# Performance work log

Hardware: AMD Instinct MI355X
Metric: run time of the kernel (lower is better)

Reference implementation:

```python
import jax, jax.numpy as jnp
import numpy as np

N = 20000        # nodes
E = 160000       # directed edges (before self loops)
NODE_DIM = 1287
HEADS = 4
C1, C2, C3 = 128, 256, 128
ACT_SLOPE = 0.15   # module's LeakyReLU between layers
GAT_SLOPE = 0.2    # PyG GATConv default negative_slope


def _gat_layer(x, src, dst, W, att_src, att_dst, bias, heads, out_dim, concat):
    # x: [N, in] ; W: [in, heads*out] ; att_*: [heads, out] ; bias: [heads*out] or [out]
    h = (x @ W).reshape(N, heads, out_dim)                      # [N, H, C]
    a_s = jnp.einsum('nhc,hc->nh', h, att_src)                  # [N, H]
    a_d = jnp.einsum('nhc,hc->nh', h, att_dst)                  # [N, H]
    e = jax.nn.leaky_relu(a_s[src] + a_d[dst], GAT_SLOPE)       # [Etot, H]
    # segment softmax over incoming edges of each dst node (self loops => no empty segments)
    m = jax.ops.segment_max(e, dst, num_segments=N)             # [N, H]
    w = jnp.exp(e - m[dst])
    den = jax.ops.segment_sum(w, dst, num_segments=N)           # [N, H]
    alpha = w / den[dst]                                        # [Etot, H]
    msg = h[src] * alpha[:, :, None]                            # [Etot, H, C]
    out = jax.ops.segment_sum(msg, dst, num_segments=N)         # [N, H, C]
    out = out.reshape(N, heads * out_dim) if concat else out.mean(axis=1)
    return out + bias


def setup_inputs() -> dict:
    key = jax.random.key(0)
    ks = jax.random.split(key, 22)
    s = 0.05
    x = jax.random.normal(ks[0], (N, NODE_DIM), jnp.float32)
    edge_index = jax.random.randint(ks[1], (2, E), 0, N, dtype=jnp.int64)
    inp = {
        'x': x, 'edge_index': edge_index,
        'W1': jax.random.normal(ks[2], (NODE_DIM, HEADS * C1), jnp.float32) * s,
        'as1': jax.random.normal(ks[3], (HEADS, C1), jnp.float32) * s,
        'ad1': jax.random.normal(ks[4], (HEADS, C1), jnp.float32) * s,
        'b1': jnp.zeros((HEADS * C1,), jnp.float32),
        'W2': jax.random.normal(ks[5], (HEADS * C1, HEADS * C2), jnp.float32) * s,
        'as2': jax.random.normal(ks[6], (HEADS, C2), jnp.float32) * s,
        'ad2': jax.random.normal(ks[7], (HEADS, C2), jnp.float32) * s,
        'b2': jnp.zeros((HEADS * C2,), jnp.float32),
        # conv3: 1024 -> 128, 1 head, no concat
        'W3': jax.random.normal(ks[8], (HEADS * C2, C3), jnp.float32) * s,
        'as3': jax.random.normal(ks[9], (1, C3), jnp.float32) * s,
        'ad3': jax.random.normal(ks[10], (1, C3), jnp.float32) * s,
        'b3': jnp.zeros((C3,), jnp.float32),
        # pre_fc: 128 -> 16
        'pw': jax.random.normal(ks[11], (C3, 16), jnp.float32) * s,
        'pb': jnp.zeros((16,), jnp.float32),
        # fc fallback: Linear(16,32) -> LeakyReLU(0.15) -> Linear(32,2)
        'f1w': jax.random.normal(ks[12], (16, 32), jnp.float32) * s,
        'f1b': jnp.zeros((32,), jnp.float32),
        'f2w': jax.random.normal(ks[13], (32, 2), jnp.float32) * s,
        'f2b': jnp.zeros((2,), jnp.float32),
    }
    return inp


def reference(x, edge_index, W1, as1, ad1, b1, W2, as2, ad2, b2,
              W3, as3, ad3, b3, pw, pb, f1w, f1b, f2w, f2b):
    loop = jnp.arange(N, dtype=edge_index.dtype)
    src = jnp.concatenate([edge_index[0], loop])   # PyG add_self_loops=True
    dst = jnp.concatenate([edge_index[1], loop])
    h = _gat_layer(x, src, dst, W1, as1, ad1, b1, HEADS, C1, True)
    h = jax.nn.leaky_relu(h, ACT_SLOPE)            # dropout = identity (eval)
    h = _gat_layer(h, src, dst, W2, as2, ad2, b2, HEADS, C2, True)
    h = jax.nn.leaky_relu(h, ACT_SLOPE)
    h = _gat_layer(h, src, dst, W3, as3, ad3, b3, 1, C3, False)
    h = jax.nn.leaky_relu(h, ACT_SLOPE)
    h = h @ pw + pb                                 # pre_fc (128 -> 16)
    h = jax.nn.leaky_relu(h @ f1w + f1b, ACT_SLOPE)
    return h @ f2w + f2b                            # [N, 2] logits
```

## Files before the change

kernel.cpp:

```cpp
#include <hip/hip_runtime.h>
#include <hip/hip_bf16.h>
#include <cstdint>
#include <cstddef>

#define LRELU(x, s) ((x) > 0.f ? (x) : (s) * (x))

typedef __attribute__((ext_vector_type(8))) short bf16x8;
typedef __attribute__((ext_vector_type(4))) float f32x4;

__device__ __forceinline__ float bflo(uint v) { return __uint_as_float(v << 16); }
__device__ __forceinline__ float bfhi(uint v) { return __uint_as_float(v & 0xffff0000u); }
__device__ __forceinline__ ushort f2bf(float f) {
  const uint u = __float_as_uint(f);
  return (ushort)((u + 0x7fffu + ((u >> 16) & 1u)) >> 16);
}

__device__ __forceinline__ void async16(const ushort* g, ushort* l) {
  __builtin_amdgcn_global_load_lds(
      (const __attribute__((address_space(1))) unsigned int*)g,
      (__attribute__((address_space(3))) unsigned int*)l, 16, 0, 0);
}

#define WAITCNT_VM(n) (0xF70 | (n))

__global__ void cast_pad_rows(const float* __restrict__ in, ushort* __restrict__ out,
                              int rows, int K, int Kp) {
  const int P4 = Kp >> 2;
  const long long idx = (long long)blockIdx.x * blockDim.x + threadIdx.x;
  if (idx >= (long long)rows * P4) return;
  const int r = (int)(idx / P4);
  const int c = ((int)(idx - (long long)r * P4)) << 2;
  const float* p = in + (size_t)r * K + c;
  float v0 = 0.f, v1 = 0.f, v2 = 0.f, v3 = 0.f;
  if (c + 3 < K) { v0 = p[0]; v1 = p[1]; v2 = p[2]; v3 = p[3]; }
  else {
    if (c + 0 < K) v0 = p[0];
    if (c + 1 < K) v1 = p[1];
    if (c + 2 < K) v2 = p[2];
    if (c + 3 < K) v3 = p[3];
  }
  uint2 o;
  o.x = (uint)f2bf(v0) | ((uint)f2bf(v1) << 16);
  o.y = (uint)f2bf(v2) | ((uint)f2bf(v3) << 16);
  *(uint2*)(out + (size_t)r * Kp + c) = o;
}

__global__ void cast_W_T(const float* __restrict__ W, ushort* __restrict__ Wt,
                         int K, int Nn, int Kp) {
  __shared__ float tile[32][33];
  const int kt = blockIdx.x * 32;
  const int nt = blockIdx.y * 32;
  const int tx = threadIdx.x;
  const int ty = threadIdx.y;
  for (int r = ty; r < 32; r += 8) {
    const int k = kt + r, nn = nt + tx;
    tile[r][tx] = (k < K && nn < Nn) ? W[(size_t)k * Nn + nn] : 0.f;
  }
  __syncthreads();
  for (int r = ty; r < 32; r += 8) {
    const int nn = nt + r, k = kt + tx;
    if (nn < Nn && k < Kp) Wt[(size_t)nn * Kp + k] = f2bf(tile[tx][r]);
  }
}

template <int TM>
__global__ __launch_bounds__(256) void gemm_bf16(
    const ushort* __restrict__ A, const ushort* __restrict__ Bt, ushort* __restrict__ C,
    int M, int N, int Kp,
    const float* __restrict__ AS, const float* __restrict__ AD,
    float* __restrict__ asb, float* __restrict__ adb, int H, int headC) {
  constexpr int MI = TM / 32;
  constexpr int LPG = (TM == 128) ? 4 : 3;
  __shared__ ushort sA[2 * TM * 32];
  __shared__ ushort sB[2 * 128 * 32];
  const int tid = threadIdx.x;
  const int wave = tid >> 6;
  const int lane = tid & 63;
  const int tilesN = N >> 7;
  const int bx = blockIdx.x % tilesN;
  const int by = blockIdx.x / tilesN;
  const int wrow = (wave >> 1) * (TM / 2);
  const int wcol = (wave & 1) * 64;
  const int quad = lane >> 4;
  const int ml = lane & 15;

  const int seg = (lane & 3) * 8;
  const int rB0 = wave * 32 + (lane >> 2);
  const int gB0 = bx * 128 + rB0;
  const ushort* pB0 = Bt + (size_t)gB0 * Kp + seg;
  const ushort* pB1 = Bt + (size_t)(gB0 + 16) * Kp + seg;
  ushort* lB0 = &sB[(wave * 32) * 32];
  ushort* lB1 = &sB[(wave * 32 + 16) * 32];
  const ushort *pA0, *pA1;
  ushort *lA0, *lA1;
  if constexpr (TM == 128) {
    const int r0 = wave * 32 + (lane >> 2);
    pA0 = A + (size_t)min(by * TM + r0, M - 1) * Kp + seg;
    pA1 = A + (size_t)min(by * TM + r0 + 16, M - 1) * Kp + seg;
    lA0 = &sA[(wave * 32) * 32];
    lA1 = &sA[(wave * 32 + 16) * 32];
  } else {
    const int r0 = wave * 16 + (lane >> 2);
    pA0 = A + (size_t)min(by * TM + r0, M - 1) * Kp + seg;
    pA1 = nullptr;
    lA0 = &sA[(wave * 16) * 32];
    lA1 = nullptr;
  }

  const int nIter = Kp >> 5;
  auto issue = [&](int it, int p) {
    const int k0 = it << 5;
    const int oa = p * TM * 32;
    const int ob_ = p * 128 * 32;
    async16(pA0 + k0, lA0 + oa);
    if constexpr (TM == 128) async16(pA1 + k0, lA1 + oa);
    async16(pB0 + k0, lB0 + ob_);
    async16(pB1 + k0, lB1 + ob_);
  };

  f32x4 acc[MI][4];
#pragma unroll
  for (int mi = 0; mi < MI; mi++)
#pragma unroll
    for (int ni = 0; ni < 4; ni++)
#pragma unroll
      for (int e = 0; e < 4; e++) acc[mi][ni][e] = 0.f;

  issue(0, 0);
  if (nIter > 1) issue(1, 1);
  int p = 0;
  for (int it = 0; it < nIter; ++it) {
    if (it + 1 < nIter) __builtin_amdgcn_s_waitcnt(WAITCNT_VM(LPG));
    else __builtin_amdgcn_s_waitcnt(WAITCNT_VM(0));
    __builtin_amdgcn_s_barrier();
    const ushort* bA = &sA[p * TM * 32];
    const ushort* bB = &sB[p * 128 * 32];
    bf16x8 af[MI], bfr[4];
#pragma unroll
    for (int mi = 0; mi < MI; mi++)
      af[mi] = *(const bf16x8*)&bA[(wrow + mi * 16 + ml) * 32 + quad * 8];
#pragma unroll
    for (int ni = 0; ni < 4; ni++)
      bfr[ni] = *(const bf16x8*)&bB[(wcol + ni * 16 + ml) * 32 + quad * 8];
#pragma unroll
    for (int mi = 0; mi < MI; mi++)
#pragma unroll
      for (int ni = 0; ni < 4; ni++)
        acc[mi][ni] = __builtin_amdgcn_mfma_f32_16x16x32_bf16(af[mi], bfr[ni], acc[mi][ni], 0, 0, 0);
    if (it + 2 < nIter) {
      __builtin_amdgcn_s_barrier();
      issue(it + 2, p);
    }
    p ^= 1;
  }

#pragma unroll
  for (int mi = 0; mi < MI; mi++) {
#pragma unroll
    for (int r = 0; r < 4; r++) {
      const int row = by * TM + wrow + mi * 16 + quad * 4 + r;
      if (row < M) {
#pragma unroll
        for (int ni = 0; ni < 4; ni++) {
          const int col = bx * 128 + wcol + ni * 16 + ml;
          C[(size_t)row * N + col] = f2bf(acc[mi][ni][r]);
        }
      }
    }
  }

  if (asb != nullptr) {
    float asv[4], adv[4];
#pragma unroll
    for (int ni = 0; ni < 4; ni++) {
      const int col = bx * 128 + wcol + ni * 16 + ml;
      asv[ni] = AS[col];
      adv[ni] = AD[col];
    }
    const int hh = (bx * 128 + wcol) / headC;
#pragma unroll
    for (int mi = 0; mi < MI; mi++) {
#pragma unroll
      for (int r = 0; r < 4; r++) {
        float ps = acc[mi][0][r] * asv[0] + acc[mi][1][r] * asv[1] +
                   acc[mi][2][r] * asv[2] + acc[mi][3][r] * asv[3];
        float pd = acc[mi][0][r] * adv[0] + acc[mi][1][r] * adv[1] +
                   acc[mi][2][r] * adv[2] + acc[mi][3][r] * adv[3];
#pragma unroll
        for (int off = 1; off < 16; off <<= 1) {
          ps += __shfl_xor(ps, off);
          pd += __shfl_xor(pd, off);
        }
        if (ml == 0) {
          const int row = by * TM + wrow + mi * 16 + quad * 4 + r;
          if (row < M) {
            atomicAdd(&asb[row * H + hh], ps);
            atomicAdd(&adb[row * H + hh], pd);
          }
        }
      }
    }
  }
}

__global__ void count_deg(const int* __restrict__ dst, int E, int* __restrict__ deg) {
  const int t = blockIdx.x * blockDim.x + threadIdx.x;
  if (t < E) atomicAdd(&deg[dst[t]], 1);
}

__global__ __launch_bounds__(1024) void scan_kernel(const int* __restrict__ deg,
                                                    int* __restrict__ rowptr,
                                                    int* __restrict__ cursor, int n) {
  __shared__ int swsum[16];
  __shared__ int carry_s;
  const int t = threadIdx.x;
  const int wv = t >> 6, lane = t & 63;
  if (t == 0) carry_s = 0;
  __syncthreads();
  for (int base = 0; base < n; base += 1024) {
    const int i = base + t;
    const int v = (i < n) ? (deg[i] + 1) : 0;
    int sc = v;
#pragma unroll
    for (int off = 1; off < 64; off <<= 1) {
      const int u = __shfl_up(sc, off);
      if (lane >= off) sc += u;
    }
    if (lane == 63) swsum[wv] = sc;
    __syncthreads();
    if (t < 16) {
      int x = swsum[t];
#pragma unroll
      for (int off = 1; off < 16; off <<= 1) {
        const int u = __shfl_up(x, off);
        if (t >= off) x += u;
      }
      swsum[t] = x;
    }
    __syncthreads();
    const int incl = sc + (wv == 0 ? 0 : swsum[wv - 1]) + carry_s;
    if (i < n) { rowptr[i + 1] = incl; cursor[i] = incl - v; }
    if (base == 0 && t == 0) rowptr[0] = 0;
    __syncthreads();
    if (t == 0) carry_s += swsum[15];
    __syncthreads();
  }
}

__global__ void scatter_edges(const int* __restrict__ esrc, const int* __restrict__ edst,
                              int E, int Etot, int* __restrict__ cursor,
                              int* __restrict__ csr_src) {
  const int t = blockIdx.x * blockDim.x + threadIdx.x;
  if (t >= Etot) return;
  int s, d;
  if (t < E) { s = esrc[t]; d = edst[t]; } else { s = t - E; d = s; }
  const int pos = atomicAdd(&cursor[d], 1);
  csr_src[pos] = s;
}

template <int H, int C>
__global__ __launch_bounds__(256) void gat_agg_wave(
    const ushort* __restrict__ hb, const int* __restrict__ rowptr,
    const int* __restrict__ csr_src, const float* __restrict__ a_s,
    const float* __restrict__ a_d, const float* __restrict__ bias,
    ushort* __restrict__ outb, float act_slope, int Nn) {
  constexpr int HC = H * C;
  constexpr int NU = HC / 2;
  constexpr int PPT = NU / 128;
  const int n = blockIdx.x * 4 + (threadIdx.x >> 6);
  const int lane = threadIdx.x & 63;
  if (n >= Nn) return;
  float ad_n[H];
#pragma unroll
  for (int h = 0; h < H; h++) ad_n[h] = a_d[n * H + h];
  const int start = rowptr[n], end = rowptr[n + 1];
  f32x4 acc[PPT];
#pragma unroll
  for (int q = 0; q < PPT; q++)
#pragma unroll
    for (int e = 0; e < 4; e++) acc[q][e] = 0.f;
  float den[H];
#pragma unroll
  for (int h = 0; h < H; h++) den[h] = 0.f;

  for (int base = start; base < end; base += 64) {
    const int cnt = min(64, end - base);
    int s = 0;
    float w[H];
#pragma unroll
    for (int h = 0; h < H; h++) w[h] = 0.f;
    if (lane < cnt) {
      s = csr_src[base + lane];
      float asv[H];
      if constexpr (H == 4) {
        const float4 t4 = *(const float4*)(a_s + s * 4);
        asv[0] = t4.x; asv[1] = t4.y; asv[2] = t4.z; asv[3] = t4.w;
      } else {
        asv[0] = a_s[s];
      }
#pragma unroll
      for (int h = 0; h < H; h++) {
        float lg = asv[h] + ad_n[h];
        lg = LRELU(lg, 0.2f);
        w[h] = __expf(lg);
        den[h] += w[h];
      }
    }
    for (int j = 0; j < cnt; j++) {
      const int sj = __shfl(s, j);
      float wj[H];
#pragma unroll
      for (int h = 0; h < H; h++) wj[h] = __shfl(w[h], j);
      const uint2* hp = (const uint2*)(hb + (size_t)sj * HC);
#pragma unroll
      for (int q = 0; q < PPT; q++) {
        const int pu = q * 128 + lane * 2;
        const uint2 v = hp[q * 64 + lane];
        const float wq = wj[(2 * pu) / C];
        acc[q][0] += wq * bflo(v.x);
        acc[q][1] += wq * bfhi(v.x);
        acc[q][2] += wq * bflo(v.y);
        acc[q][3] += wq * bfhi(v.y);
      }
    }
  }
#pragma unroll
  for (int h = 0; h < H; h++) {
#pragma unroll
    for (int off = 1; off < 64; off <<= 1) den[h] += __shfl_xor(den[h], off);
    den[h] = 1.f / den[h];
  }
#pragma unroll
  for (int q = 0; q < PPT; q++) {
    const int pu = q * 128 + lane * 2;
    const float iv = den[(2 * pu) / C];
    const float4 b4 = *(const float4*)(bias + 2 * pu);
    const float o0 = LRELU(acc[q][0] * iv + b4.x, act_slope);
    const float o1 = LRELU(acc[q][1] * iv + b4.y, act_slope);
    const float o2 = LRELU(acc[q][2] * iv + b4.z, act_slope);
    const float o3 = LRELU(acc[q][3] * iv + b4.w, act_slope);
    uint2 o;
    o.x = (uint)f2bf(o0) | ((uint)f2bf(o1) << 16);
    o.y = (uint)f2bf(o2) | ((uint)f2bf(o3) << 16);
    ((uint2*)outb)[(size_t)n * (NU / 2) + q * 64 + lane] = o;
  }
}

__global__ __launch_bounds__(64) void gat_agg3_mlp(
    const ushort* __restrict__ hb, const int* __restrict__ rowptr,
    const int* __restrict__ csr_src, const float* __restrict__ a_s,
    const float* __restrict__ a_d, const float* __restrict__ b3,
    const float* __restrict__ pw, const float* __restrict__ pb,
    const float* __restrict__ f1w, const float* __restrict__ f1b,
    const float* __restrict__ f2w, const float* __restrict__ f2b,
    float* __restrict__ out) {
  const int n = blockIdx.x;
  const int tid = threadIdx.x;
  __shared__ float sx[128];
  __shared__ float s1[16];
  __shared__ float s2[32];
  const float ad_n = a_d[n];
  const int start = rowptr[n], end = rowptr[n + 1];
  float2 acc = make_float2(0.f, 0.f);
  float den = 0.f;
  for (int base = start; base < end; base += 64) {
    const int cnt = min(64, end - base);
    int s = 0;
    float w = 0.f;
    if (tid < cnt) {
      s = csr_src[base + tid];
      float lg = a_s[s] + ad_n;
      lg = LRELU(lg, 0.2f);
      w = __expf(lg);
      den += w;
    }
    for (int j = 0; j < cnt; j++) {
      const int sj = __shfl(s, j);
      const float wj = __shfl(w, j);
      const uint v = ((const uint*)(hb + (size_t)sj * 128))[tid];
      acc.x += wj * bflo(v);
      acc.y += wj * bfhi(v);
    }
  }
#pragma unroll
  for (int off = 1; off < 64; off <<= 1) den += __shfl_xor(den, off);
  const float iv = 1.f / den;
  sx[2 * tid]     = LRELU(acc.x * iv + b3[2 * tid], 0.15f);
  sx[2 * tid + 1] = LRELU(acc.y * iv + b3[2 * tid + 1], 0.15f);
  __syncthreads();
  if (tid < 16) {
    float a = pb[tid];
    for (int c = 0; c < 128; c++) a += sx[c] * pw[c * 16 + tid];
    s1[tid] = a;
  }
  __syncthreads();
  if (tid < 32) {
    float a = f1b[tid];
    for (int c = 0; c < 16; c++) a += s1[c] * f1w[c * 32 + tid];
    s2[tid] = LRELU(a, 0.15f);
  }
  __syncthreads();
  if (tid < 2) {
    float a = f2b[tid];
    for (int c = 0; c < 32; c++) a += s2[c] * f2w[c * 2 + tid];
    out[(size_t)n * 2 + tid] = a;
  }
}

extern "C" void kernel_launch(void* const* d_in, const int* in_sizes, int n_in,
                              void* d_out, int out_size, void* d_ws, size_t ws_size,
                              hipStream_t stream) {
  const float* x   = (const float*)d_in[0];
  const int* ei    = (const int*)d_in[1];
  const float* W1  = (const float*)d_in[2];
  const float* as1 = (const float*)d_in[3];
  const float* ad1 = (const float*)d_in[4];
  const float* b1  = (const float*)d_in[5];
  const float* W2  = (const float*)d_in[6];
  const float* as2 = (const float*)d_in[7];
  const float* ad2 = (const float*)d_in[8];
  const float* b2  = (const float*)d_in[9];
  const float* W3  = (const float*)d_in[10];
  const float* as3 = (const float*)d_in[11];
  const float* ad3 = (const float*)d_in[12];
  const float* b3  = (const float*)d_in[13];
  const float* pw  = (const float*)d_in[14];
  const float* pb  = (const float*)d_in[15];
  const float* f1w = (const float*)d_in[16];
  const float* f1b = (const float*)d_in[17];
  const float* f2w = (const float*)d_in[18];
  const float* f2b = (const float*)d_in[19];
  float* out = (float*)d_out;

  const int N = in_sizes[0] / 1287;
  const int E = in_sizes[1] / 2;
  const int Etot = E + N;
  const int* esrc = ei;
  const int* edst = ei + E;
  const int K1 = 1287, K1p = 1312;

  char* ws = (char*)d_ws;
  size_t off = 0;
  auto alloc = [&](size_t bytes) -> void* {
    void* p = ws + off;
    off = (off + bytes + 255) & ~(size_t)255;
    return p;
  };
  ushort* hb  = (ushort*)alloc((size_t)N * 1024 * 2);
  ushort* ob  = (ushort*)alloc((size_t)N * 1024 * 2);
  ushort* xb  = (ushort*)alloc((size_t)N * K1p * 2);
  ushort* W1t = (ushort*)alloc((size_t)512 * K1p * 2);
  ushort* W2t = (ushort*)alloc((size_t)1024 * 512 * 2);
  ushort* W3t = (ushort*)alloc((size_t)128 * 1024 * 2);
  float* av   = (float*)alloc((size_t)N * 8 * sizeof(float));
  int* deg    = (int*)alloc((size_t)N * sizeof(int));
  int* rowptr = (int*)alloc((size_t)(N + 1) * sizeof(int));
  int* cursor = (int*)alloc((size_t)N * sizeof(int));
  int* csr    = (int*)alloc((size_t)Etot * sizeof(int));
  float* asb = av;
  float* adb = av + (size_t)N * 4;

  hipMemsetAsync(deg, 0, (size_t)N * sizeof(int), stream);
  count_deg<<<(E + 255) / 256, 256, 0, stream>>>(edst, E, deg);
  scan_kernel<<<1, 1024, 0, stream>>>(deg, rowptr, cursor, N);
  scatter_edges<<<(Etot + 255) / 256, 256, 0, stream>>>(esrc, edst, E, Etot, cursor, csr);

  {
    const long long nx = (long long)N * (K1p / 4);
    cast_pad_rows<<<(int)((nx + 255) / 256), 256, 0, stream>>>(x, xb, N, K1, K1p);
    cast_W_T<<<dim3(K1p / 32, (512 + 31) / 32), dim3(32, 8), 0, stream>>>(W1, W1t, K1, 512, K1p);
    cast_W_T<<<dim3(512 / 32, 1024 / 32), dim3(32, 8), 0, stream>>>(W2, W2t, 512, 1024, 512);
    cast_W_T<<<dim3(1024 / 32, 128 / 32), dim3(32, 8), 0, stream>>>(W3, W3t, 1024, 128, 1024);
  }

  const int tilesM = (N + 127) / 128;
  const int tilesM64 = (N + 63) / 64;
  const int aggBlocks = (N + 3) / 4;

  {
    const int H = 4, C = 128, HC = 512;
    hipMemsetAsync(av, 0, (size_t)N * 8 * sizeof(float), stream);
    gemm_bf16<128><<<tilesM * (HC / 128), 256, 0, stream>>>(xb, W1t, hb, N, HC, K1p,
                                                            as1, ad1, asb, adb, H, C);
    gat_agg_wave<4, 128><<<aggBlocks, 256, 0, stream>>>(hb, rowptr, csr, asb, adb,
                                                        b1, ob, 0.15f, N);
  }
  {
    const int H = 4, C = 256, HC = 1024;
    hipMemsetAsync(av, 0, (size_t)N * 8 * sizeof(float), stream);
    gemm_bf16<128><<<tilesM * (HC / 128), 256, 0, stream>>>(ob, W2t, hb, N, HC, 512,
                                                            as2, ad2, asb, adb, H, C);
    gat_agg_wave<4, 256><<<aggBlocks, 256, 0, stream>>>(hb, rowptr, csr, asb, adb,
                                                        b2, ob, 0.15f, N);
  }
  {
    const int HC = 128;
    hipMemsetAsync(av, 0, (size_t)N * 8 * sizeof(float), stream);
    gemm_bf16<64><<<tilesM64 * (HC / 128), 256, 0, stream>>>(ob, W3t, hb, N, HC, 1024,
                                                             as3, ad3, asb, adb, 1, 128);
    gat_agg3_mlp<<<N, 64, 0, stream>>>(hb, rowptr, csr, asb, adb, b3,
                                       pw, pb, f1w, f1b, f2w, f2b, out);
  }
}
```

Baseline: 524.1 us.

## Swizzle GEMM LDS layout, remap blocks per XCD, widen aggregation loads

The GEMM now XOR-swizzles the 16-byte segment position in LDS, applying the same swizzle on write and read, to reduce bank conflicts on the bf16x8 fragment reads. It also remaps workgroup IDs so that consecutive tiles land on the same XCD, improving L2 reuse of A and B tiles. Separately, the aggregation kernel switches from 8-byte to 16-byte per-lane gathers of neighbor features, halving the load instruction count. The wider gather requires HC to be a multiple of 512 (true for layers 1 and 2) and keeps each lane's 8 elements within one head.

```diff
diff --git a/kernel.cpp b/kernel.cpp
--- a/kernel.cpp
+++ b/kernel.cpp
@@ -77,14 +77,19 @@
   const int wave = tid >> 6;
   const int lane = tid & 63;
   const int tilesN = N >> 7;
-  const int bx = blockIdx.x % tilesN;
-  const int by = blockIdx.x / tilesN;
+  const int nwg = gridDim.x;
+  const int q8 = nwg >> 3, r8 = nwg & 7;
+  const int xcd = blockIdx.x & 7;
+  const int lid = blockIdx.x >> 3;
+  const int wg = (xcd < r8 ? xcd * (q8 + 1) : r8 * (q8 + 1) + (xcd - r8) * q8) + lid;
+  const int bx = wg % tilesN;
+  const int by = wg / tilesN;
   const int wrow = (wave >> 1) * (TM / 2);
   const int wcol = (wave & 1) * 64;
   const int quad = lane >> 4;
   const int ml = lane & 15;
 
-  const int seg = (lane & 3) * 8;
+  const int seg = (((lane & 3) ^ ((lane >> 3) & 3)) * 8);
   const int rB0 = wave * 32 + (lane >> 2);
   const int gB0 = bx * 128 + rB0;
   const ushort* pB0 = Bt + (size_t)gB0 * Kp + seg;
@@ -126,6 +131,8 @@
 #pragma unroll
       for (int e = 0; e < 4; e++) acc[mi][ni][e] = 0.f;
 
+  const int rq = (quad ^ ((ml >> 1) & 3)) * 8;
+
   issue(0, 0);
   if (nIter > 1) issue(1, 1);
   int p = 0;
@@ -138,10 +145,10 @@
     bf16x8 af[MI], bfr[4];
 #pragma unroll
     for (int mi = 0; mi < MI; mi++)
-      af[mi] = *(const bf16x8*)&bA[(wrow + mi * 16 + ml) * 32 + quad * 8];
+      af[mi] = *(const bf16x8*)&bA[(wrow + mi * 16 + ml) * 32 + rq];
 #pragma unroll
     for (int ni = 0; ni < 4; ni++)
-      bfr[ni] = *(const bf16x8*)&bB[(wcol + ni * 16 + ml) * 32 + quad * 8];
+      bfr[ni] = *(const bf16x8*)&bB[(wcol + ni * 16 + ml) * 32 + rq];
 #pragma unroll
     for (int mi = 0; mi < MI; mi++)
 #pragma unroll
@@ -266,7 +273,7 @@
     ushort* __restrict__ outb, float act_slope, int Nn) {
   constexpr int HC = H * C;
   constexpr int NU = HC / 2;
-  constexpr int PPT = NU / 128;
+  constexpr int UPT = NU / 256;
   const int n = blockIdx.x * 4 + (threadIdx.x >> 6);
   const int lane = threadIdx.x & 63;
   if (n >= Nn) return;
@@ -274,11 +281,13 @@
 #pragma unroll
   for (int h = 0; h < H; h++) ad_n[h] = a_d[n * H + h];
   const int start = rowptr[n], end = rowptr[n + 1];
-  f32x4 acc[PPT];
-#pragma unroll
-  for (int q = 0; q < PPT; q++)
-#pragma unroll
-    for (int e = 0; e < 4; e++) acc[q][e] = 0.f;
+  f32x4 acc[UPT][2];
+#pragma unroll
+  for (int q = 0; q < UPT; q++)
+#pragma unroll
+    for (int u = 0; u < 2; u++)
+#pragma unroll
+      for (int e = 0; e < 4; e++) acc[q][u][e] = 0.f;
   float den[H];
 #pragma unroll
   for (int h = 0; h < H; h++) den[h] = 0.f;
@@ -311,16 +320,20 @@
       float wj[H];
 #pragma unroll
       for (int h = 0; h < H; h++) wj[h] = __shfl(w[h], j);
-      const uint2* hp = (const uint2*)(hb + (size_t)sj * HC);
-#pragma unroll
-      for (int q = 0; q < PPT; q++) {
-        const int pu = q * 128 + lane * 2;
-        const uint2 v = hp[q * 64 + lane];
-        const float wq = wj[(2 * pu) / C];
-        acc[q][0] += wq * bflo(v.x);
-        acc[q][1] += wq * bfhi(v.x);
-        acc[q][2] += wq * bflo(v.y);
-        acc[q][3] += wq * bfhi(v.y);
+      const uint4* hp = (const uint4*)(hb + (size_t)sj * HC);
+#pragma unroll
+      for (int q = 0; q < UPT; q++) {
+        const int e0 = q * 512 + 8 * lane;
+        const uint4 v = hp[q * 64 + lane];
+        const float wq = wj[e0 / C];
+        acc[q][0][0] += wq * bflo(v.x);
+        acc[q][0][1] += wq * bfhi(v.x);
+        acc[q][0][2] += wq * bflo(v.y);
+        acc[q][0][3] += wq * bfhi(v.y);
+        acc[q][1][0] += wq * bflo(v.z);
+        acc[q][1][1] += wq * bfhi(v.z);
+        acc[q][1][2] += wq * bflo(v.w);
+        acc[q][1][3] += wq * bfhi(v.w);
       }
     }
   }
@@ -331,18 +344,25 @@
     den[h] = 1.f / den[h];
   }
 #pragma unroll
-  for (int q = 0; q < PPT; q++) {
-    const int pu = q * 128 + lane * 2;
-    const float iv = den[(2 * pu) / C];
-    const float4 b4 = *(const float4*)(bias + 2 * pu);
-    const float o0 = LRELU(acc[q][0] * iv + b4.x, act_slope);
-    const float o1 = LRELU(acc[q][1] * iv + b4.y, act_slope);
-    const float o2 = LRELU(acc[q][2] * iv + b4.z, act_slope);
-    const float o3 = LRELU(acc[q][3] * iv + b4.w, act_slope);
-    uint2 o;
+  for (int q = 0; q < UPT; q++) {
+    const int e0 = q * 512 + 8 * lane;
+    const float iv = den[e0 / C];
+    const float4 ba = *(const float4*)(bias + e0);
+    const float4 bb = *(const float4*)(bias + e0 + 4);
+    const float o0 = LRELU(acc[q][0][0] * iv + ba.x, act_slope);
+    const float o1 = LRELU(acc[q][0][1] * iv + ba.y, act_slope);
+    const float o2 = LRELU(acc[q][0][2] * iv + ba.z, act_slope);
+    const float o3 = LRELU(acc[q][0][3] * iv + ba.w, act_slope);
+    const float o4 = LRELU(acc[q][1][0] * iv + bb.x, act_slope);
+    const float o5 = LRELU(acc[q][1][1] * iv + bb.y, act_slope);
+    const float o6 = LRELU(acc[q][1][2] * iv + bb.z, act_slope);
+    const float o7 = LRELU(acc[q][1][3] * iv + bb.w, act_slope);
+    uint4 o;
     o.x = (uint)f2bf(o0) | ((uint)f2bf(o1) << 16);
     o.y = (uint)f2bf(o2) | ((uint)f2bf(o3) << 16);
-    ((uint2*)outb)[(size_t)n * (NU / 2) + q * 64 + lane] = o;
+    o.z = (uint)f2bf(o4) | ((uint)f2bf(o5) << 16);
+    o.w = (uint)f2bf(o6) | ((uint)f2bf(o7) << 16);
+    ((uint4*)outb)[(size_t)n * (NU / 4) + q * 64 + lane] = o;
   }
 }
 
```

Result: no change. 515.7 us (-1.6%).
